# Kernel tuning notes

Measured on AMD Instinct MI355X. Metric: run time of the kernel, lower is better.

Reference implementation:

```python
import jax, jax.numpy as jnp
import numpy as np

B, T, I, H = 4096, 256, 6, 64


def _gru_layer(x, W_ih, W_hh, b_ih, b_hh):
    # x: [B,T,Din]; W_ih: [3H,Din]; W_hh: [3H,H]
    xg = jnp.einsum('btd,gd->btg', x, W_ih) + b_ih  # [B,T,3H] input projections
    xg = jnp.transpose(xg, (1, 0, 2))               # [T,B,3H] for scan
    h0 = jnp.zeros((x.shape[0], H), dtype=x.dtype)

    def step(h, xg_t):
        hg = h @ W_hh.T + b_hh                      # [B,3H]
        xr, xz, xn = jnp.split(xg_t, 3, axis=-1)
        hr, hz, hn = jnp.split(hg, 3, axis=-1)
        r = jax.nn.sigmoid(xr + hr)
        z = jax.nn.sigmoid(xz + hz)
        n = jnp.tanh(xn + r * hn)
        h_new = (1.0 - z) * n + z * h
        return h_new, h_new

    _, hs = jax.lax.scan(step, h0, xg)              # hs: [T,B,H]
    return jnp.transpose(hs, (1, 0, 2))             # [B,T,H]


def setup_inputs() -> dict:
    key = jax.random.key(0)
    ks = jax.random.split(key, 11)
    s_i0 = 1.0 / np.sqrt(H)
    u = lambda k, shape: jax.random.uniform(k, shape, jnp.float32, -s_i0, s_i0)
    return {
        'x': jax.random.normal(ks[0], (B, T, I), dtype=jnp.float32),
        'W_ih0': u(ks[1], (3 * H, I)),
        'W_hh0': u(ks[2], (3 * H, H)),
        'b_ih0': u(ks[3], (3 * H,)),
        'b_hh0': u(ks[4], (3 * H,)),
        'W_ih1': u(ks[5], (3 * H, H)),
        'W_hh1': u(ks[6], (3 * H, H)),
        'b_ih1': u(ks[7], (3 * H,)),
        'b_hh1': u(ks[8], (3 * H,)),
        'W_fc': u(ks[9], (1, H)),
        'b_fc': u(ks[10], (1,)),
    }


def reference(x, W_ih0, W_hh0, b_ih0, b_hh0, W_ih1, W_hh1, b_ih1, b_hh1, W_fc, b_fc):
    h1 = _gru_layer(x, W_ih0, W_hh0, b_ih0, b_hh0)   # [B,T,H]
    h2 = _gru_layer(h1, W_ih1, W_hh1, b_ih1, b_hh1)  # [B,T,H]
    last = h2[:, -1, :]                              # [B,H] (dropout is identity in eval)
    out = last @ W_fc.T + b_fc                       # [B,1]
    return out[:, 0]                                 # squeeze(-1) -> [B]
```

## Files before the change

kernel.cpp:

```cpp
#include <hip/hip_runtime.h>
#include <stdint.h>

#define TT 256
#define II 6
#define HH 64
#define MB 16

typedef __attribute__((ext_vector_type(8))) _Float16 half8;
typedef __attribute__((ext_vector_type(4))) float f32x4;

#define K_LOG2E  1.44269504f
#define K_2LOG2E 2.88539008f

#define BAR() asm volatile("s_waitcnt lgkmcnt(0)\n\ts_barrier" ::: "memory")

static __device__ __forceinline__ uint32_t pkh(float a, float b){
    uint16_t ha = __builtin_bit_cast(uint16_t, (_Float16)a);
    uint16_t hb = __builtin_bit_cast(uint16_t, (_Float16)b);
    return (uint32_t)ha | ((uint32_t)hb << 16);
}
static __device__ __forceinline__ uint32_t pkrtz(float a, float b){
    return __builtin_bit_cast(uint32_t, __builtin_amdgcn_cvt_pkrtz(a, b));
}
static __device__ __forceinline__ half8 mkh8(uint32_t a, uint32_t b, uint32_t c, uint32_t d){
    union { uint32_t u[4]; half8 v; } x;
    x.u[0]=a; x.u[1]=b; x.u[2]=c; x.u[3]=d;
    return x.v;
}
static __device__ __forceinline__ half8 ldq(const uint32_t* p){
    union { uint4 q; half8 v; } x;
    x.q = *(const uint4*)p;
    return x.v;
}
static __device__ __forceinline__ f32x4 MFi(half8 A, half8 B, f32x4 C){
    return __builtin_amdgcn_mfma_f32_16x16x32_f16(A, B, C, 0, 0, 0);
}

static __device__ __forceinline__ uint2 gates(const f32x4& Cr, const f32x4& Cz,
                                              const f32x4& Cxn, const f32x4& Chn,
                                              f32x4& hp)
{
    float num[4], den[4], zg4[4];
    #pragma unroll
    for (int q = 0; q < 4; ++q){
        float er = __builtin_amdgcn_exp2f(-Cr[q]);
        float ez = __builtin_amdgcn_exp2f(-Cz[q]);
        float pa = 1.0f + er, pb = 1.0f + ez;
        float u  = __builtin_amdgcn_rcpf(pa * pb);
        float rg = u * pb;
        zg4[q]   = u * pa;
        float v  = Cxn[q] + rg * Chn[q];
        float e  = __builtin_amdgcn_exp2f(-v);
        num[q] = 1.0f - e;
        den[q] = 1.0f + e;
    }
    float hn[4];
    #pragma unroll
    for (int pr = 0; pr < 2; ++pr){
        const int q0 = 2*pr, q1 = 2*pr + 1;
        float t  = __builtin_amdgcn_rcpf(den[q0] * den[q1]);
        float n0 = num[q0] * (t * den[q1]);
        float n1 = num[q1] * (t * den[q0]);
        float h0 = n0 + zg4[q0] * (hp[q0] - n0);
        float h1 = n1 + zg4[q1] * (hp[q1] - n1);
        hp[q0] = h0; hp[q1] = h1;
        hn[q0] = h0; hn[q1] = h1;
    }
    return make_uint2(pkrtz(hn[0], hn[1]), pkrtz(hn[2], hn[3]));
}

__global__ __launch_bounds__(512, 2)
void gru2_v9(const float* __restrict__ x,
             const float* __restrict__ Wih0, const float* __restrict__ Whh0,
             const float* __restrict__ bih0, const float* __restrict__ bhh0,
             const float* __restrict__ Wih1, const float* __restrict__ Whh1,
             const float* __restrict__ bih1, const float* __restrict__ bhh1,
             const float* __restrict__ Wfc,  const float* __restrict__ bfc,
             float* __restrict__ out)
{
    __shared__ uint32_t h0buf[2][MB][36];
    __shared__ uint32_t h1buf[2][MB][36];
    __shared__ float    fcpart[16][MB];

    const int tid  = threadIdx.x;
    const int lane = tid & 63;
    const int wg   = tid >> 6;
    const int isL1 = (wg >= 4);
    const int w    = wg & 3;
    const int c    = lane >> 4;
    const int r16  = lane & 15;
    const int b0   = blockIdx.x * MB;

    for (int i = tid; i < 2 * MB * 36; i += 512){
        (&h0buf[0][0][0])[i] = 0u;
        (&h1buf[0][0][0])[i] = 0u;
    }

    const float gsc[3] = { K_LOG2E, K_LOG2E, K_2LOG2E };
    half8 AW[6][2];
    {
        const float* M0 = isL1 ? Wih1 : Whh0;
        #pragma unroll
        for (int m = 0; m < 6; ++m){
            if (m >= 3 && !isL1) continue;
            const float* Wb = (m < 3) ? M0 : Whh1;
            const float s = gsc[m % 3];
            const float* rowp = Wb + (size_t)((m % 3) * 64 + w * 16 + r16) * HH;
            #pragma unroll
            for (int cw = 0; cw < 2; ++cw){
                const float* pp = rowp + cw * 32 + c * 8;
                AW[m][cw] = mkh8(pkh(s*pp[0], s*pp[1]), pkh(s*pp[2], s*pp[3]),
                                 pkh(s*pp[4], s*pp[5]), pkh(s*pp[6], s*pp[7]));
            }
        }
    }
    half8 Ax[3];
    #pragma unroll
    for (int g = 0; g < 3; ++g){
        if (c == 0 && !isL1){
            const float s = gsc[g];
            const float* rowp = Wih0 + (size_t)(g * 64 + w * 16 + r16) * II;
            Ax[g] = mkh8(pkh(s*rowp[0], s*rowp[1]), pkh(s*rowp[2], s*rowp[3]),
                         pkh(s*rowp[4], s*rowp[5]), 0u);
        } else {
            Ax[g] = mkh8(0u, 0u, 0u, 0u);
        }
    }

    const float* bi = isL1 ? bih1 : bih0;
    const float* bh = isL1 ? bhh1 : bhh0;
    const int rq0 = w * 16 + c * 4;
    f32x4 Br, Bz, Bxn, Bhn;
    #pragma unroll
    for (int q = 0; q < 4; ++q){
        Br[q]  = K_LOG2E  * (bi[      rq0 + q] + bh[      rq0 + q]);
        Bz[q]  = K_LOG2E  * (bi[ 64 + rq0 + q] + bh[ 64 + rq0 + q]);
        Bxn[q] = K_2LOG2E *  bi[128 + rq0 + q];
        Bhn[q] = K_2LOG2E *  bh[128 + rq0 + q];
    }

    f32x4 hp = {0.f, 0.f, 0.f, 0.f};

    const uint32_t* rd0[2] = { &h0buf[0][r16][4*c], &h0buf[1][r16][4*c] };
    const uint32_t* rd1[2] = { &h1buf[0][r16][4*c], &h1buf[1][r16][4*c] };
    uint2* wr0[2] = { (uint2*)&h0buf[0][r16][8*w + 2*c], (uint2*)&h0buf[1][r16][8*w + 2*c] };
    uint2* wr1[2] = { (uint2*)&h1buf[0][r16][8*w + 2*c], (uint2*)&h1buf[1][r16][8*w + 2*c] };

    f32x4 Pr = {0,0,0,0}, Pz = {0,0,0,0}, Pxn = {0,0,0,0};

    const float* xq = nullptr;
    float2 x0v, x1v, x2v;
    if (!isL1){
        xq = x + (size_t)(b0 + r16) * (TT * II);
        float2 a  = *(const float2*)(xq + 0);
        float2 bb = *(const float2*)(xq + 2);
        float2 cc = *(const float2*)(xq + 4);
        half8 XB = mkh8(pkrtz(a.x, a.y), pkrtz(bb.x, bb.y), pkrtz(cc.x, cc.y), 0u);
        Pr  = MFi(Ax[0], XB, Br);
        Pz  = MFi(Ax[1], XB, Bz);
        Pxn = MFi(Ax[2], XB, Bxn);
        xq += II;
        x0v = *(const float2*)(xq + 0);
        x1v = *(const float2*)(xq + 2);
        x2v = *(const float2*)(xq + 4);
    }
    __syncthreads();

#define L0TICK(P, TK) do {                                                          \
    half8 H0 = ldq(rd0[P]);                                                         \
    half8 H1 = ldq(rd0[P] + 16);                                                    \
    __builtin_amdgcn_s_setprio(1);                                                  \
    f32x4 Cr  = MFi(AW[0][0], H0, Pr);   f32x4 Cz  = MFi(AW[1][0], H0, Pz);         \
    Cr        = MFi(AW[0][1], H1, Cr);   Cz        = MFi(AW[1][1], H1, Cz);         \
    f32x4 Chn = MFi(AW[2][0], H0, Bhn);  Chn       = MFi(AW[2][1], H1, Chn);        \
    __builtin_amdgcn_s_setprio(0);                                                  \
    uint2 d = gates(Cr, Cz, Pxn, Chn, hp);                                          \
    *wr0[(P) ^ 1] = d;                                                              \
    if ((TK) + 1 < TT){         \
        half8 XB = mkh8(pkrtz(x0v.x, x0v.y), pkrtz(x1v.x, x1v.y),                   \
                        pkrtz(x2v.x, x2v.y), 0u);                                   \
        Pr  = MFi(Ax[0], XB, Br);                                                   \
        Pz  = MFi(Ax[1], XB, Bz);                                                   \
        Pxn = MFi(Ax[2], XB, Bxn);                                                  \
        if ((TK) + 2 < TT){                                                         \
            xq += II;                                                               \
            x0v = *(const float2*)(xq + 0);                                         \
            x1v = *(const float2*)(xq + 2);                                         \
            x2v = *(const float2*)(xq + 4);                                         \
        }                                                                           \
    }                                                                               \
} while(0)

#define L1TICK(P) do {                                                              \
    half8 G0 = ldq(rd0[P]);                                                         \
    half8 G1 = ldq(rd0[P] + 16);                                                    \
    half8 H0 = ldq(rd1[P]);                                                         \
    half8 H1 = ldq(rd1[P] + 16);                                                    \
    __builtin_amdgcn_s_setprio(1);                                                  \
    f32x4 Cr  = MFi(AW[0][0], G0, Br);   f32x4 Cz  = MFi(AW[1][0], G0, Bz);         \
    Cr        = MFi(AW[0][1], G1, Cr);   Cz        = MFi(AW[1][1], G1, Cz);         \
    Cr        = MFi(AW[3][0], H0, Cr);   Cz        = MFi(AW[4][0], H0, Cz);         \
    Cr        = MFi(AW[3][1], H1, Cr);   Cz        = MFi(AW[4][1], H1, Cz);         \
    f32x4 Cxn = MFi(AW[2][0], G0, Bxn);  Cxn       = MFi(AW[2][1], G1, Cxn);        \
    f32x4 Chn = MFi(AW[5][0], H0, Bhn);  Chn       = MFi(AW[5][1], H1, Chn);        \
    __builtin_amdgcn_s_setprio(0);                                                  \
    uint2 d = gates(Cr, Cz, Cxn, Chn, hp);                                          \
    *wr1[(P) ^ 1] = d;                                                              \
} while(0)

    if (!isL1) L0TICK(0, 0);
    BAR();
    #pragma unroll 1
    for (int tk = 1; tk < 255; tk += 2){
        if (!isL1) L0TICK(1, tk); else L1TICK(1);
        BAR();
        if (!isL1) L0TICK(0, tk + 1); else L1TICK(0);
        BAR();
    }
    if (!isL1) L0TICK(1, 255); else L1TICK(1);
    BAR();
    if (isL1) L1TICK(0);

#undef L0TICK
#undef L1TICK

    if (isL1){
        float4 wf = *(const float4*)(Wfc + w * 16 + c * 4);
        fcpart[w * 4 + c][r16] =
            hp[0] * wf.x + hp[1] * wf.y + hp[2] * wf.z + hp[3] * wf.w;
    }
    __syncthreads();
    if (tid < MB){
        float s = bfc[0];
        #pragma unroll
        for (int k = 0; k < 16; ++k) s += fcpart[k][tid];
        out[b0 + tid] = s;
    }
}

extern "C" void kernel_launch(void* const* d_in, const int* in_sizes, int n_in,
                              void* d_out, int out_size, void* d_ws, size_t ws_size,
                              hipStream_t stream)
{
    const float* x    = (const float*)d_in[0];
    const float* Wih0 = (const float*)d_in[1];
    const float* Whh0 = (const float*)d_in[2];
    const float* bih0 = (const float*)d_in[3];
    const float* bhh0 = (const float*)d_in[4];
    const float* Wih1 = (const float*)d_in[5];
    const float* Whh1 = (const float*)d_in[6];
    const float* bih1 = (const float*)d_in[7];
    const float* bhh1 = (const float*)d_in[8];
    const float* Wfc  = (const float*)d_in[9];
    const float* bfc  = (const float*)d_in[10];
    float* out = (float*)d_out;

    dim3 grid(4096 / MB), block(512);
    gru2_v9<<<grid, block, 0, stream>>>(x, Wih0, Whh0, bih0, bhh0,
                                        Wih1, Whh1, bih1, bhh1,
                                        Wfc, bfc, out);
}
```

Measured before the change: 135.8 us.

## Split each GRU layer's gates across two wave groups with LDS handoff

Doubles the block to 1024 threads so each layer has two roles: one set of waves computes the r/z gate MFMAs and sigmoids and writes them to shared memory, the other computes the n-gate MFMAs, reads r/z back and finishes tanh and the hidden-state update. The aim is to shorten the per-timestep critical path by spreading the MFMA and transcendental work over more waves. In exchange every timestep now needs two barriers instead of one, adds an LDS round trip for the gate values, and doubles the threads per block, which reduces how many blocks can be resident.

```diff
diff --git a/kernel.cpp b/kernel.cpp
--- a/kernel.cpp
+++ b/kernel.cpp
@@ -35,22 +35,30 @@
 static __device__ __forceinline__ f32x4 MFi(half8 A, half8 B, f32x4 C){
     return __builtin_amdgcn_mfma_f32_16x16x32_f16(A, B, C, 0, 0, 0);
 }
-
-static __device__ __forceinline__ uint2 gates(const f32x4& Cr, const f32x4& Cz,
-                                              const f32x4& Cxn, const f32x4& Chn,
-                                              f32x4& hp)
-{
-    float num[4], den[4], zg4[4];
+union U4F { uint4 u; f32x4 f; };
+
+static __device__ __forceinline__ void sigma_store(const f32x4& Cr, const f32x4& Cz,
+                                                   uint4* pR, uint4* pZ){
+    U4F rg, zg;
     #pragma unroll
     for (int q = 0; q < 4; ++q){
         float er = __builtin_amdgcn_exp2f(-Cr[q]);
         float ez = __builtin_amdgcn_exp2f(-Cz[q]);
         float pa = 1.0f + er, pb = 1.0f + ez;
         float u  = __builtin_amdgcn_rcpf(pa * pb);
-        float rg = u * pb;
-        zg4[q]   = u * pa;
-        float v  = Cxn[q] + rg * Chn[q];
-        float e  = __builtin_amdgcn_exp2f(-v);
+        rg.f[q] = u * pb;
+        zg.f[q] = u * pa;
+    }
+    *pR = rg.u; *pZ = zg.u;
+}
+static __device__ __forceinline__ uint2 finish_n(const f32x4& Cxn, const f32x4& Chn,
+                                                 uint4 rgu, uint4 zgu, f32x4& hp){
+    U4F rg, zg; rg.u = rgu; zg.u = zgu;
+    float num[4], den[4];
+    #pragma unroll
+    for (int q = 0; q < 4; ++q){
+        float v = Cxn[q] + rg.f[q] * Chn[q];
+        float e = __builtin_amdgcn_exp2f(-v);
         num[q] = 1.0f - e;
         den[q] = 1.0f + e;
     }
@@ -61,104 +69,156 @@
         float t  = __builtin_amdgcn_rcpf(den[q0] * den[q1]);
         float n0 = num[q0] * (t * den[q1]);
         float n1 = num[q1] * (t * den[q0]);
-        float h0 = n0 + zg4[q0] * (hp[q0] - n0);
-        float h1 = n1 + zg4[q1] * (hp[q1] - n1);
+        float h0 = n0 + zg.f[q0] * (hp[q0] - n0);
+        float h1 = n1 + zg.f[q1] * (hp[q1] - n1);
         hp[q0] = h0; hp[q1] = h1;
         hn[q0] = h0; hn[q1] = h1;
     }
     return make_uint2(pkrtz(hn[0], hn[1]), pkrtz(hn[2], hn[3]));
 }
 
-__global__ __launch_bounds__(512, 2)
-void gru2_v9(const float* __restrict__ x,
-             const float* __restrict__ Wih0, const float* __restrict__ Whh0,
-             const float* __restrict__ bih0, const float* __restrict__ bhh0,
-             const float* __restrict__ Wih1, const float* __restrict__ Whh1,
-             const float* __restrict__ bih1, const float* __restrict__ bhh1,
-             const float* __restrict__ Wfc,  const float* __restrict__ bfc,
-             float* __restrict__ out)
+__global__ __launch_bounds__(1024, 4)
+void gru2_v11(const float* __restrict__ x,
+              const float* __restrict__ Wih0, const float* __restrict__ Whh0,
+              const float* __restrict__ bih0, const float* __restrict__ bhh0,
+              const float* __restrict__ Wih1, const float* __restrict__ Whh1,
+              const float* __restrict__ bih1, const float* __restrict__ bhh1,
+              const float* __restrict__ Wfc,  const float* __restrict__ bfc,
+              float* __restrict__ out)
 {
     __shared__ uint32_t h0buf[2][MB][36];
     __shared__ uint32_t h1buf[2][MB][36];
+    __shared__ uint4    rgb[2][4][64];
+    __shared__ uint4    zgb[2][4][64];
     __shared__ float    fcpart[16][MB];
 
-    const int tid  = threadIdx.x;
-    const int lane = tid & 63;
-    const int wg   = tid >> 6;
-    const int isL1 = (wg >= 4);
-    const int w    = wg & 3;
-    const int c    = lane >> 4;
-    const int r16  = lane & 15;
-    const int b0   = blockIdx.x * MB;
-
-    for (int i = tid; i < 2 * MB * 36; i += 512){
+    const int tid   = threadIdx.x;
+    const int lane  = tid & 63;
+    const int wg    = tid >> 6;
+    const int layer = wg >> 3;
+    const int role  = (wg >> 2) & 1;
+    const int w     = wg & 3;
+    const int c     = lane >> 4;
+    const int r16   = lane & 15;
+    const int b0    = blockIdx.x * MB;
+
+    for (int i = tid; i < 2 * MB * 36; i += 1024){
         (&h0buf[0][0][0])[i] = 0u;
         (&h1buf[0][0][0])[i] = 0u;
     }
 
-    const float gsc[3] = { K_LOG2E, K_LOG2E, K_2LOG2E };
-    half8 AW[6][2];
-    {
-        const float* M0 = isL1 ? Wih1 : Whh0;
+    half8 WA[2][2];
+    half8 WB[2][2];
+    half8 WN1[2];
+    half8 WN2[2];
+    half8 AxA[2], AxN;
+    f32x4 B1, B2;
+
+    const int rq0 = w * 16 + c * 4;
+    const float* bi = layer ? bih1 : bih0;
+    const float* bh = layer ? bhh1 : bhh0;
+    if (role == 0){
+        const float* Wp = layer ? Wih1 : Whh0;
         #pragma unroll
-        for (int m = 0; m < 6; ++m){
-            if (m >= 3 && !isL1) continue;
-            const float* Wb = (m < 3) ? M0 : Whh1;
-            const float s = gsc[m % 3];
-            const float* rowp = Wb + (size_t)((m % 3) * 64 + w * 16 + r16) * HH;
+        for (int g = 0; g < 2; ++g){
+            const float* rowp = Wp + (size_t)(g * 64 + w * 16 + r16) * HH;
             #pragma unroll
             for (int cw = 0; cw < 2; ++cw){
                 const float* pp = rowp + cw * 32 + c * 8;
-                AW[m][cw] = mkh8(pkh(s*pp[0], s*pp[1]), pkh(s*pp[2], s*pp[3]),
-                                 pkh(s*pp[4], s*pp[5]), pkh(s*pp[6], s*pp[7]));
-            }
-        }
-    }
-    half8 Ax[3];
-    #pragma unroll
-    for (int g = 0; g < 3; ++g){
-        if (c == 0 && !isL1){
-            const float s = gsc[g];
-            const float* rowp = Wih0 + (size_t)(g * 64 + w * 16 + r16) * II;
-            Ax[g] = mkh8(pkh(s*rowp[0], s*rowp[1]), pkh(s*rowp[2], s*rowp[3]),
-                         pkh(s*rowp[4], s*rowp[5]), 0u);
+                WA[g][cw] = mkh8(pkh(K_LOG2E*pp[0], K_LOG2E*pp[1]),
+                                 pkh(K_LOG2E*pp[2], K_LOG2E*pp[3]),
+                                 pkh(K_LOG2E*pp[4], K_LOG2E*pp[5]),
+                                 pkh(K_LOG2E*pp[6], K_LOG2E*pp[7]));
+            }
+        }
+        if (layer){
+            #pragma unroll
+            for (int g = 0; g < 2; ++g){
+                const float* rowp = Whh1 + (size_t)(g * 64 + w * 16 + r16) * HH;
+                #pragma unroll
+                for (int cw = 0; cw < 2; ++cw){
+                    const float* pp = rowp + cw * 32 + c * 8;
+                    WB[g][cw] = mkh8(pkh(K_LOG2E*pp[0], K_LOG2E*pp[1]),
+                                     pkh(K_LOG2E*pp[2], K_LOG2E*pp[3]),
+                                     pkh(K_LOG2E*pp[4], K_LOG2E*pp[5]),
+                                     pkh(K_LOG2E*pp[6], K_LOG2E*pp[7]));
+                }
+            }
         } else {
-            Ax[g] = mkh8(0u, 0u, 0u, 0u);
-        }
-    }
-
-    const float* bi = isL1 ? bih1 : bih0;
-    const float* bh = isL1 ? bhh1 : bhh0;
-    const int rq0 = w * 16 + c * 4;
-    f32x4 Br, Bz, Bxn, Bhn;
-    #pragma unroll
-    for (int q = 0; q < 4; ++q){
-        Br[q]  = K_LOG2E  * (bi[      rq0 + q] + bh[      rq0 + q]);
-        Bz[q]  = K_LOG2E  * (bi[ 64 + rq0 + q] + bh[ 64 + rq0 + q]);
-        Bxn[q] = K_2LOG2E *  bi[128 + rq0 + q];
-        Bhn[q] = K_2LOG2E *  bh[128 + rq0 + q];
-    }
-
-    f32x4 hp = {0.f, 0.f, 0.f, 0.f};
+            #pragma unroll
+            for (int g = 0; g < 2; ++g){
+                if (c == 0){
+                    const float* rowp = Wih0 + (size_t)(g * 64 + w * 16 + r16) * II;
+                    AxA[g] = mkh8(pkh(K_LOG2E*rowp[0], K_LOG2E*rowp[1]),
+                                  pkh(K_LOG2E*rowp[2], K_LOG2E*rowp[3]),
+                                  pkh(K_LOG2E*rowp[4], K_LOG2E*rowp[5]), 0u);
+                } else AxA[g] = mkh8(0u,0u,0u,0u);
+            }
+        }
+        #pragma unroll
+        for (int q = 0; q < 4; ++q){
+            B1[q] = K_LOG2E * (bi[     rq0 + q] + bh[     rq0 + q]);
+            B2[q] = K_LOG2E * (bi[64 + rq0 + q] + bh[64 + rq0 + q]);
+        }
+    } else {
+        const float* Wp = layer ? Wih1 : Whh0;
+        {
+            const float* rowp = Wp + (size_t)(128 + w * 16 + r16) * HH;
+            #pragma unroll
+            for (int cw = 0; cw < 2; ++cw){
+                const float* pp = rowp + cw * 32 + c * 8;
+                WN1[cw] = mkh8(pkh(K_2LOG2E*pp[0], K_2LOG2E*pp[1]),
+                               pkh(K_2LOG2E*pp[2], K_2LOG2E*pp[3]),
+                               pkh(K_2LOG2E*pp[4], K_2LOG2E*pp[5]),
+                               pkh(K_2LOG2E*pp[6], K_2LOG2E*pp[7]));
+            }
+        }
+        if (layer){
+            const float* rowp = Whh1 + (size_t)(128 + w * 16 + r16) * HH;
+            #pragma unroll
+            for (int cw = 0; cw < 2; ++cw){
+                const float* pp = rowp + cw * 32 + c * 8;
+                WN2[cw] = mkh8(pkh(K_2LOG2E*pp[0], K_2LOG2E*pp[1]),
+                               pkh(K_2LOG2E*pp[2], K_2LOG2E*pp[3]),
+                               pkh(K_2LOG2E*pp[4], K_2LOG2E*pp[5]),
+                               pkh(K_2LOG2E*pp[6], K_2LOG2E*pp[7]));
+            }
+        } else {
+            if (c == 0){
+                const float* rowp = Wih0 + (size_t)(128 + w * 16 + r16) * II;
+                AxN = mkh8(pkh(K_2LOG2E*rowp[0], K_2LOG2E*rowp[1]),
+                           pkh(K_2LOG2E*rowp[2], K_2LOG2E*rowp[3]),
+                           pkh(K_2LOG2E*rowp[4], K_2LOG2E*rowp[5]), 0u);
+            } else AxN = mkh8(0u,0u,0u,0u);
+        }
+        #pragma unroll
+        for (int q = 0; q < 4; ++q){
+            B1[q] = K_2LOG2E * bi[128 + rq0 + q];
+            B2[q] = K_2LOG2E * bh[128 + rq0 + q];
+        }
+    }
 
     const uint32_t* rd0[2] = { &h0buf[0][r16][4*c], &h0buf[1][r16][4*c] };
     const uint32_t* rd1[2] = { &h1buf[0][r16][4*c], &h1buf[1][r16][4*c] };
-    uint2* wr0[2] = { (uint2*)&h0buf[0][r16][8*w + 2*c], (uint2*)&h0buf[1][r16][8*w + 2*c] };
-    uint2* wr1[2] = { (uint2*)&h1buf[0][r16][8*w + 2*c], (uint2*)&h1buf[1][r16][8*w + 2*c] };
-
-    f32x4 Pr = {0,0,0,0}, Pz = {0,0,0,0}, Pxn = {0,0,0,0};
+    uint32_t* hwr = layer ? &h1buf[0][r16][8*w + 2*c] : &h0buf[0][r16][8*w + 2*c];
+    uint2* wrp[2] = { (uint2*)hwr, (uint2*)(hwr + MB*36) };
+    uint4* sgR = &rgb[layer][w][lane];
+    uint4* sgZ = &zgb[layer][w][lane];
+
+    f32x4 hp  = {0.f,0.f,0.f,0.f};
+    f32x4 Pr  = {0.f,0.f,0.f,0.f}, Pz = Pr, Pxn = Pr;
+    f32x4 Cxn = Pr, Chn = Pr;
 
     const float* xq = nullptr;
-    float2 x0v, x1v, x2v;
-    if (!isL1){
+    float2 x0v = make_float2(0.f,0.f), x1v = x0v, x2v = x0v;
+    if (layer == 0){
         xq = x + (size_t)(b0 + r16) * (TT * II);
         float2 a  = *(const float2*)(xq + 0);
         float2 bb = *(const float2*)(xq + 2);
         float2 cc = *(const float2*)(xq + 4);
         half8 XB = mkh8(pkrtz(a.x, a.y), pkrtz(bb.x, bb.y), pkrtz(cc.x, cc.y), 0u);
-        Pr  = MFi(Ax[0], XB, Br);
-        Pz  = MFi(Ax[1], XB, Bz);
-        Pxn = MFi(Ax[2], XB, Bxn);
+        if (role == 0){ Pr = MFi(AxA[0], XB, B1); Pz = MFi(AxA[1], XB, B2); }
+        else          { Pxn = MFi(AxN, XB, B1); }
         xq += II;
         x0v = *(const float2*)(xq + 0);
         x1v = *(const float2*)(xq + 2);
@@ -166,65 +226,94 @@
     }
     __syncthreads();
 
-#define L0TICK(P, TK) do {                                                          \
-    half8 H0 = ldq(rd0[P]);                                                         \
-    half8 H1 = ldq(rd0[P] + 16);                                                    \
-    __builtin_amdgcn_s_setprio(1);                                                  \
-    f32x4 Cr  = MFi(AW[0][0], H0, Pr);   f32x4 Cz  = MFi(AW[1][0], H0, Pz);         \
-    Cr        = MFi(AW[0][1], H1, Cr);   Cz        = MFi(AW[1][1], H1, Cz);         \
-    f32x4 Chn = MFi(AW[2][0], H0, Bhn);  Chn       = MFi(AW[2][1], H1, Chn);        \
-    __builtin_amdgcn_s_setprio(0);                                                  \
-    uint2 d = gates(Cr, Cz, Pxn, Chn, hp);                                          \
-    *wr0[(P) ^ 1] = d;                                                              \
-    if ((TK) + 1 < TT){         \
-        half8 XB = mkh8(pkrtz(x0v.x, x0v.y), pkrtz(x1v.x, x1v.y),                   \
-                        pkrtz(x2v.x, x2v.y), 0u);                                   \
-        Pr  = MFi(Ax[0], XB, Br);                                                   \
-        Pz  = MFi(Ax[1], XB, Bz);                                                   \
-        Pxn = MFi(Ax[2], XB, Bxn);                                                  \
-        if ((TK) + 2 < TT){                                                         \
-            xq += II;                                                               \
-            x0v = *(const float2*)(xq + 0);                                         \
-            x1v = *(const float2*)(xq + 2);                                         \
-            x2v = *(const float2*)(xq + 4);                                         \
+#define PHA(P, TK) do {                                                             \
+    if (layer == 0){ if ((TK) < TT){                                                \
+        half8 H0 = ldq(rd0[P]); half8 H1 = ldq(rd0[P] + 16);                        \
+        if (role == 0){                                                             \
+            __builtin_amdgcn_s_setprio(1);                                          \
+            f32x4 Cr = MFi(WA[0][0], H0, Pr); Cr = MFi(WA[0][1], H1, Cr);           \
+            f32x4 Cz = MFi(WA[1][0], H0, Pz); Cz = MFi(WA[1][1], H1, Cz);           \
+            __builtin_amdgcn_s_setprio(0);                                          \
+            sigma_store(Cr, Cz, sgR, sgZ);                                          \
+        } else {                                                                    \
+            __builtin_amdgcn_s_setprio(1);                                          \
+            Chn = MFi(WN1[0], H0, B2); Chn = MFi(WN1[1], H1, Chn);                  \
+            __builtin_amdgcn_s_setprio(0);                                          \
+            Cxn = Pxn;                                                              \
+        }                                                                           \
+    }} else { if ((TK) >= 1){                                                       \
+        half8 G0 = ldq(rd0[P]); half8 G1 = ldq(rd0[P] + 16);                        \
+        half8 H0 = ldq(rd1[P]); half8 H1 = ldq(rd1[P] + 16);                        \
+        if (role == 0){                                                             \
+            __builtin_amdgcn_s_setprio(1);                                          \
+            f32x4 Cr = MFi(WA[0][0], G0, B1); Cr = MFi(WA[0][1], G1, Cr);           \
+            Cr = MFi(WB[0][0], H0, Cr);       Cr = MFi(WB[0][1], H1, Cr);           \
+            f32x4 Cz = MFi(WA[1][0], G0, B2); Cz = MFi(WA[1][1], G1, Cz);           \
+            Cz = MFi(WB[1][0], H0, Cz);       Cz = MFi(WB[1][1], H1, Cz);           \
+            __builtin_amdgcn_s_setprio(0);                                          \
+            sigma_store(Cr, Cz, sgR, sgZ);                                          \
+        } else {                                                                    \
+            __builtin_amdgcn_s_setprio(1);                                          \
+            Cxn = MFi(WN1[0], G0, B1); Cxn = MFi(WN1[1], G1, Cxn);                  \
+            Chn = MFi(WN2[0], H0, B2); Chn = MFi(WN2[1], H1, Chn);                  \
+            __builtin_amdgcn_s_setprio(0);                                          \
+        }                                                                           \
+    }}                                                                              \
+} while(0)
+
+#define PHB(P, TK) do {                                                             \
+    if (role == 1){                                                                 \
+        const bool act = (layer == 0) ? ((TK) < TT) : ((TK) >= 1);                  \
+        if (act){                                                                   \
+            uint4 rgu = *sgR; uint4 zgu = *sgZ;                                     \
+            uint2 d = finish_n(Cxn, Chn, rgu, zgu, hp);                             \
+            *wrp[(P) ^ 1] = d;                                                      \
+        }                                                                           \
+        if (layer == 0 && (TK) + 1 < TT){                                           \
+            half8 XB = mkh8(pkrtz(x0v.x, x0v.y), pkrtz(x1v.x, x1v.y),               \
+                            pkrtz(x2v.x, x2v.y), 0u);                               \
+            Pxn = MFi(AxN, XB, B1);                                                 \
+            if ((TK) + 2 < TT){                                                     \
+                xq += II;                                                           \
+                x0v = *(const float2*)(xq + 0);                                     \
+                x1v = *(const float2*)(xq + 2);                                     \
+                x2v = *(const float2*)(xq + 4);                                     \
+            }                                                                       \
+        }                                                                           \
+    } else {                                                                        \
+        if (layer == 0 && (TK) + 1 < TT){                                           \
+            half8 XB = mkh8(pkrtz(x0v.x, x0v.y), pkrtz(x1v.x, x1v.y),               \
+                            pkrtz(x2v.x, x2v.y), 0u);                               \
+            Pr = MFi(AxA[0], XB, B1);                                               \
+            Pz = MFi(AxA[1], XB, B2);                                               \
+            if ((TK) + 2 < TT){                                                     \
+                xq += II;                                                           \
+                x0v = *(const float2*)(xq + 0);                                     \
+                x1v = *(const float2*)(xq + 2);                                     \
+                x2v = *(const float2*)(xq + 4);                                     \
+            }                                                                       \
         }                                                                           \
     }                                                                               \
 } while(0)
 
-#define L1TICK(P) do {                                                              \
-    half8 G0 = ldq(rd0[P]);                                                         \
-    half8 G1 = ldq(rd0[P] + 16);                                                    \
-    half8 H0 = ldq(rd1[P]);                                                         \
-    half8 H1 = ldq(rd1[P] + 16);                                                    \
-    __builtin_amdgcn_s_setprio(1);                                                  \
-    f32x4 Cr  = MFi(AW[0][0], G0, Br);   f32x4 Cz  = MFi(AW[1][0], G0, Bz);         \
-    Cr        = MFi(AW[0][1], G1, Cr);   Cz        = MFi(AW[1][1], G1, Cz);         \
-    Cr        = MFi(AW[3][0], H0, Cr);   Cz        = MFi(AW[4][0], H0, Cz);         \
-    Cr        = MFi(AW[3][1], H1, Cr);   Cz        = MFi(AW[4][1], H1, Cz);         \
-    f32x4 Cxn = MFi(AW[2][0], G0, Bxn);  Cxn       = MFi(AW[2][1], G1, Cxn);        \
-    f32x4 Chn = MFi(AW[5][0], H0, Bhn);  Chn       = MFi(AW[5][1], H1, Chn);        \
-    __builtin_amdgcn_s_setprio(0);                                                  \
-    uint2 d = gates(Cr, Cz, Cxn, Chn, hp);                                          \
-    *wr1[(P) ^ 1] = d;                                                              \
-} while(0)
-
-    if (!isL1) L0TICK(0, 0);
-    BAR();
+    PHA(0, 0);  BAR();
+    PHB(0, 0);  BAR();
     #pragma unroll 1
     for (int tk = 1; tk < 255; tk += 2){
-        if (!isL1) L0TICK(1, tk); else L1TICK(1);
-        BAR();
-        if (!isL1) L0TICK(0, tk + 1); else L1TICK(0);
-        BAR();
-    }
-    if (!isL1) L0TICK(1, 255); else L1TICK(1);
-    BAR();
-    if (isL1) L1TICK(0);
-
-#undef L0TICK
-#undef L1TICK
-
-    if (isL1){
+        PHA(1, tk);     BAR();
+        PHB(1, tk);     BAR();
+        PHA(0, tk + 1); BAR();
+        PHB(0, tk + 1); BAR();
+    }
+    PHA(1, 255); BAR();
+    PHB(1, 255); BAR();
+    PHA(0, 256); BAR();
+    PHB(0, 256);
+
+#undef PHA
+#undef PHB
+
+    if (layer == 1 && role == 1){
         float4 wf = *(const float4*)(Wfc + w * 16 + c * 4);
         fcpart[w * 4 + c][r16] =
             hp[0] * wf.x + hp[1] * wf.y + hp[2] * wf.z + hp[3] * wf.w;
@@ -255,8 +344,8 @@
     const float* bfc  = (const float*)d_in[10];
     float* out = (float*)d_out;
 
-    dim3 grid(4096 / MB), block(512);
-    gru2_v9<<<grid, block, 0, stream>>>(x, Wih0, Whh0, bih0, bhh0,
-                                        Wih1, Whh1, bih1, bhh1,
-                                        Wfc, bfc, out);
-}
+    dim3 grid(4096 / MB), block(1024);
+    gru2_v11<<<grid, block, 0, stream>>>(x, Wih0, Whh0, bih0, bhh0,
+                                         Wih1, Whh1, bih1, bhh1,
+                                         Wfc, bfc, out);
+}
```

New measurement: 350.6 us. 2.58x slower.
